# Optimization experiments

Measured on AMD Instinct MI355X. Metric: run time of the kernel, lower is better.

Reference implementation:

```python
import jax, jax.numpy as jnp
import numpy as np

NUM_EMBEDDINGS = 8192
EMB_CHANNELS = 8
BETA = 0.25


def setup_inputs() -> dict:
    key = jax.random.key(0)
    k1, k2 = jax.random.split(key)
    z = jax.random.normal(k1, (8, EMB_CHANNELS, 64, 64), dtype=jnp.float32)
    # torch init: uniform(-1/K, 1/K)
    lim = 1.0 / NUM_EMBEDDINGS
    codebook = jax.random.uniform(
        k2, (NUM_EMBEDDINGS, EMB_CHANNELS), dtype=jnp.float32,
        minval=-lim, maxval=lim)
    return {"z": z, "codebook": codebook}


def reference(z, codebook):
    # z: [B, C, H, W]; codebook: [K, C]
    C = codebook.shape[1]
    z_ch = jnp.moveaxis(z, 1, -1)                 # [B, H, W, C]
    z_flat = z_ch.reshape(-1, C)                  # [N, C]
    # squared-euclidean distances via sum-of-squares + matmul: [N, K]
    dist = (
        jnp.sum(z_flat ** 2, axis=1, keepdims=True)
        + jnp.sum(codebook ** 2, axis=1)
        - 2.0 * jnp.einsum('nd,kd->nk', z_flat, codebook)
    )
    idx = jnp.argmin(dist, axis=1)                # [N]
    z_q = codebook[idx].reshape(z_ch.shape)       # [B, H, W, C]
    z_q = jnp.moveaxis(z_q, -1, 1)                # [B, C, H, W]
    sg = jax.lax.stop_gradient
    loss = (BETA * jnp.mean((sg(z_q) - z) ** 2)
            + jnp.mean((z_q - sg(z)) ** 2))
    # straight-through estimator
    z_q_st = z + sg(z_q - z)
    return z_q_st, loss
```

## Files before the change

kernel.cpp:

```cpp
#include <hip/hip_runtime.h>

typedef __attribute__((ext_vector_type(8))) short short8;
typedef __attribute__((ext_vector_type(4))) float f32x4;

#define NROWS 32768
#define NELEM 262144
#define KCB   8192
#define ROWS_PB 128
#define NWAVE 16

static __device__ __forceinline__ short to_bf16(float x) {
    unsigned u = __float_as_uint(x);
    unsigned r = (u + 0x7FFFu + ((u >> 16) & 1u)) >> 16;
    return (short)r;
}

__global__ __launch_bounds__(256) void vq_prep(
    const float* __restrict__ z, const float* __restrict__ cb,
    short8* __restrict__ cbb, short8* __restrict__ pka, float* __restrict__ out)
{
    int gid = blockIdx.x * 256 + threadIdx.x;
    if (gid == 0) out[NELEM] = 0.0f;
    if (gid < KCB) {
        const float4* p = (const float4*)(cb + (size_t)gid * 8);
        float4 a = p[0], b = p[1];
        float h = -0.5f * (a.x*a.x + a.y*a.y + a.z*a.z + a.w*a.w
                         + b.x*b.x + b.y*b.y + b.z*b.z + b.w*b.w);
        short8 lo = { to_bf16(a.x), to_bf16(a.y), to_bf16(a.z), to_bf16(a.w),
                      to_bf16(b.x), to_bf16(b.y), to_bf16(b.z), to_bf16(b.w) };
        short8 hi = { to_bf16(h), 0, 0, 0, 0, 0, 0, 0 };
        cbb[2 * gid]     = lo;
        cbb[2 * gid + 1] = hi;
    } else {
        int n = gid - KCB;
        int bb = n >> 12, hw = n & 4095;
        const float* zp = z + (size_t)bb * 32768 + hw;
        short8 v = { to_bf16(zp[0]),     to_bf16(zp[4096]),
                     to_bf16(zp[8192]),  to_bf16(zp[12288]),
                     to_bf16(zp[16384]), to_bf16(zp[20480]),
                     to_bf16(zp[24576]), to_bf16(zp[28672]) };
        pka[n] = v;
    }
}

__global__ __launch_bounds__(1024, 4) void vq_main(
    const float* __restrict__ z, const float* __restrict__ cb,
    const short8* __restrict__ cbb, const short8* __restrict__ pka,
    float* __restrict__ out)
{
    __shared__ float sbest[NWAVE][ROWS_PB];
    __shared__ float lsum[NWAVE];

    const int tid  = threadIdx.x;
    const int lane = tid & 63;
    const int w    = tid >> 6;
    const int col  = lane & 15;
    const int g    = lane >> 4;

    const int row0 = blockIdx.x * ROWS_PB;

    short8 af[8];
    #pragma unroll
    for (int f = 0; f < 8; ++f) {
        short8 v = {0, 0, 0, 0, 0, 0, 0, 0};
        if (g == 0)      v = pka[row0 + f * 16 + col];
        else if (g == 1) v[0] = (short)0x3F80;
        af[f] = v;
    }

    const int kbase = w * (KCB / NWAVE);
    const char* bpc = (const char*)cbb + (size_t)(kbase + col) * 32
                                       + (size_t)(g & 1) * 16;

    float best[8][4];
    #pragma unroll
    for (int f = 0; f < 8; ++f)
        #pragma unroll
        for (int r = 0; r < 4; ++r)
            best[f][r] = __uint_as_float(0xFF800000u);

    const unsigned inv0 = (unsigned)(8191 - (kbase + col));
    const f32x4 zacc = {0.f, 0.f, 0.f, 0.f};

#define LDT(T) (*(const short8*)(bpc + (size_t)(T) * 512))

    auto comp = [&](short8 bf, int t) {
        unsigned iv = inv0 - (unsigned)(t * 16);
        #pragma unroll
        for (int f = 0; f < 8; ++f) {
            f32x4 acc = __builtin_amdgcn_mfma_f32_16x16x32_bf16(af[f], bf, zacc, 0, 0, 0);
            #pragma unroll
            for (int r = 0; r < 4; ++r) {
                float p = __uint_as_float((__float_as_uint(acc[r]) & 0xFFFFE000u) | iv);
                best[f][r] = fmaxf(best[f][r], p);
            }
        }
    };

    short8 c0 = LDT(0);
    short8 c1 = LDT(1);
    #pragma unroll
    for (int tt = 0; tt < 16; ++tt) {
        short8 n0, n1;
        if (tt < 15) { n0 = LDT(2 * tt + 2); n1 = LDT(2 * tt + 3); }
        comp(c0, 2 * tt);
        comp(c1, 2 * tt + 1);
        if (tt < 15) { c0 = n0; c1 = n1; }
    }

    #pragma unroll
    for (int d = 1; d < 16; d <<= 1)
        #pragma unroll
        for (int f = 0; f < 8; ++f)
            #pragma unroll
            for (int r = 0; r < 4; ++r)
                best[f][r] = fmaxf(best[f][r], __shfl_xor(best[f][r], d));

    if (col == 0) {
        #pragma unroll
        for (int f = 0; f < 8; ++f)
            #pragma unroll
            for (int r = 0; r < 4; ++r)
                sbest[w][f * 16 + g * 4 + r] = best[f][r];
    }
    __syncthreads();

    const int pos = tid & 127;
    const int ch  = tid >> 7;
    float m = sbest[0][pos];
    #pragma unroll
    for (int kw = 1; kw < NWAVE; ++kw) m = fmaxf(m, sbest[kw][pos]);
    const int k = 8191 - (int)(__float_as_uint(m) & 8191u);

    const int n = row0 + pos;
    const size_t o = ((size_t)(n >> 12)) * 32768 + (size_t)ch * 4096 + (size_t)(n & 4095);
    float ev = cb[(size_t)k * 8 + ch];
    float zz = z[o];
    out[o] = ev;
    float dd = ev - zz;
    float sq = dd * dd;
    #pragma unroll
    for (int off = 32; off > 0; off >>= 1) sq += __shfl_down(sq, off);
    if (lane == 0) lsum[w] = sq;
    __syncthreads();
    if (tid == 0) {
        float s = 0.f;
        #pragma unroll
        for (int kw = 0; kw < NWAVE; ++kw) s += lsum[kw];
        atomicAdd(out + NELEM, s * (1.25f / (float)NELEM));
    }
}

extern "C" void kernel_launch(void* const* d_in, const int* in_sizes, int n_in,
                              void* d_out, int out_size, void* d_ws, size_t ws_size,
                              hipStream_t stream)
{
    const float* z  = (const float*)d_in[0];
    const float* cb = (const float*)d_in[1];
    float* out = (float*)d_out;
    short8* cbb = (short8*)d_ws;
    short8* pka = (short8*)((char*)d_ws + 256 * 1024);

    vq_prep<<<(KCB + NROWS) / 256, 256, 0, stream>>>(z, cb, cbb, pka, out);
    vq_main<<<NROWS / ROWS_PB, 1024, 0, stream>>>(z, cb, cbb, pka, out);
}
```

Before: 39.48 us.

## Switch VQ distance scan to 32x32x16 MFMA with fused and-or/max3 argmax

Replaces the 16x16x32 MFMA tiling, where half of each A operand was padding, with 32x32x16 MFMAs. The codebook is re-laid out in 32-entry blocks that carry separate low and high K halves, so the A operand holds 32 rows plus a bias column and the MFMA produces more useful output per instruction. The argmax packing now uses inline v_and_or_b32 and v_max3_f32 to halve the compare-and-max instruction count per pair of tiles. Blocks shrink to 32 rows and 8 waves, giving 1024 blocks instead of 256. Each block therefore reloads the whole codebook for fewer rows, which means less reuse and more L2 traffic.

```diff
diff --git a/kernel.cpp b/kernel.cpp
--- a/kernel.cpp
+++ b/kernel.cpp
@@ -1,13 +1,13 @@
 #include <hip/hip_runtime.h>
 
 typedef __attribute__((ext_vector_type(8))) short short8;
-typedef __attribute__((ext_vector_type(4))) float f32x4;
+typedef __attribute__((ext_vector_type(16))) float f32x16;
 
 #define NROWS 32768
 #define NELEM 262144
 #define KCB   8192
-#define ROWS_PB 128
-#define NWAVE 16
+#define ROWS_PB 32
+#define NWAVE 8
 
 static __device__ __forceinline__ short to_bf16(float x) {
     unsigned u = __float_as_uint(x);
@@ -17,7 +17,7 @@
 
 __global__ __launch_bounds__(256) void vq_prep(
     const float* __restrict__ z, const float* __restrict__ cb,
-    short8* __restrict__ cbb, short8* __restrict__ pka, float* __restrict__ out)
+    short8* __restrict__ cbb32, short8* __restrict__ pka, float* __restrict__ out)
 {
     int gid = blockIdx.x * 256 + threadIdx.x;
     if (gid == 0) out[NELEM] = 0.0f;
@@ -29,8 +29,8 @@
         short8 lo = { to_bf16(a.x), to_bf16(a.y), to_bf16(a.z), to_bf16(a.w),
                       to_bf16(b.x), to_bf16(b.y), to_bf16(b.z), to_bf16(b.w) };
         short8 hi = { to_bf16(h), 0, 0, 0, 0, 0, 0, 0 };
-        cbb[2 * gid]     = lo;
-        cbb[2 * gid + 1] = hi;
+        cbb32[(gid >> 5) * 64 + (gid & 31)]      = lo;
+        cbb32[(gid >> 5) * 64 + 32 + (gid & 31)] = hi;
     } else {
         int n = gid - KCB;
         int bb = n >> 12, hw = n & 4095;
@@ -43,9 +43,21 @@
     }
 }
 
-__global__ __launch_bounds__(1024, 4) void vq_main(
+static __device__ __forceinline__ void packmax3(float& best, float s0, float s1,
+                                                unsigned iv0, unsigned iv1)
+{
+    float p0, p1;
+    asm("v_and_or_b32 %0, %1, %2, %3"
+        : "=v"(p0) : "v"(s0), "s"(0xFFFFE000u), "v"(iv0));
+    asm("v_and_or_b32 %0, %1, %2, %3"
+        : "=v"(p1) : "v"(s1), "s"(0xFFFFE000u), "v"(iv1));
+    asm("v_max3_f32 %0, %1, %2, %0"
+        : "+v"(best) : "v"(p0), "v"(p1));
+}
+
+__global__ __launch_bounds__(512, 4) void vq_scan32(
     const float* __restrict__ z, const float* __restrict__ cb,
-    const short8* __restrict__ cbb, const short8* __restrict__ pka,
+    const short8* __restrict__ cbb32, const short8* __restrict__ pka,
     float* __restrict__ out)
 {
     __shared__ float sbest[NWAVE][ROWS_PB];
@@ -54,91 +66,79 @@
     const int tid  = threadIdx.x;
     const int lane = tid & 63;
     const int w    = tid >> 6;
-    const int col  = lane & 15;
-    const int g    = lane >> 4;
+    const int c32  = lane & 31;
+    const int hi   = lane >> 5;
 
     const int row0 = blockIdx.x * ROWS_PB;
 
-    short8 af[8];
-    #pragma unroll
-    for (int f = 0; f < 8; ++f) {
-        short8 v = {0, 0, 0, 0, 0, 0, 0, 0};
-        if (g == 0)      v = pka[row0 + f * 16 + col];
-        else if (g == 1) v[0] = (short)0x3F80;
-        af[f] = v;
+    short8 af;
+    if (hi == 0) {
+        af = pka[row0 + c32];
+    } else {
+        short8 one = {(short)0x3F80, 0, 0, 0, 0, 0, 0, 0};
+        af = one;
     }
 
     const int kbase = w * (KCB / NWAVE);
-    const char* bpc = (const char*)cbb + (size_t)(kbase + col) * 32
-                                       + (size_t)(g & 1) * 16;
+    const char* bpc = (const char*)cbb32 + (size_t)kbase * 32
+                    + (size_t)c32 * 16 + (size_t)hi * 512;
 
-    float best[8][4];
+    float best[16];
     #pragma unroll
-    for (int f = 0; f < 8; ++f)
+    for (int r = 0; r < 16; ++r)
+        best[r] = __uint_as_float(0xFF800000u);
+
+    const unsigned inv0 = 8191u - (unsigned)kbase - (unsigned)c32;
+    const f32x16 z16 = {0.f,0.f,0.f,0.f,0.f,0.f,0.f,0.f,
+                        0.f,0.f,0.f,0.f,0.f,0.f,0.f,0.f};
+
+    #pragma unroll 4
+    for (int pr = 0; pr < 16; ++pr) {
+        const char* p = bpc + (size_t)pr * 2048;
+        short8 b0 = *(const short8*)(p);
+        short8 b1 = *(const short8*)(p + 1024);
+        f32x16 d0 = __builtin_amdgcn_mfma_f32_32x32x16_bf16(af, b0, z16, 0, 0, 0);
+        f32x16 d1 = __builtin_amdgcn_mfma_f32_32x32x16_bf16(af, b1, z16, 0, 0, 0);
+        const unsigned iv0 = inv0 - (unsigned)(pr * 64);
+        const unsigned iv1 = iv0 - 32u;
         #pragma unroll
-        for (int r = 0; r < 4; ++r)
-            best[f][r] = __uint_as_float(0xFF800000u);
-
-    const unsigned inv0 = (unsigned)(8191 - (kbase + col));
-    const f32x4 zacc = {0.f, 0.f, 0.f, 0.f};
-
-#define LDT(T) (*(const short8*)(bpc + (size_t)(T) * 512))
-
-    auto comp = [&](short8 bf, int t) {
-        unsigned iv = inv0 - (unsigned)(t * 16);
-        #pragma unroll
-        for (int f = 0; f < 8; ++f) {
-            f32x4 acc = __builtin_amdgcn_mfma_f32_16x16x32_bf16(af[f], bf, zacc, 0, 0, 0);
-            #pragma unroll
-            for (int r = 0; r < 4; ++r) {
-                float p = __uint_as_float((__float_as_uint(acc[r]) & 0xFFFFE000u) | iv);
-                best[f][r] = fmaxf(best[f][r], p);
-            }
-        }
-    };
-
-    short8 c0 = LDT(0);
-    short8 c1 = LDT(1);
-    #pragma unroll
-    for (int tt = 0; tt < 16; ++tt) {
-        short8 n0, n1;
-        if (tt < 15) { n0 = LDT(2 * tt + 2); n1 = LDT(2 * tt + 3); }
-        comp(c0, 2 * tt);
-        comp(c1, 2 * tt + 1);
-        if (tt < 15) { c0 = n0; c1 = n1; }
+        for (int r = 0; r < 16; ++r)
+            packmax3(best[r], d0[r], d1[r], iv0, iv1);
     }
 
     #pragma unroll
-    for (int d = 1; d < 16; d <<= 1)
+    for (int d = 1; d < 32; d <<= 1)
         #pragma unroll
-        for (int f = 0; f < 8; ++f)
-            #pragma unroll
-            for (int r = 0; r < 4; ++r)
-                best[f][r] = fmaxf(best[f][r], __shfl_xor(best[f][r], d));
+        for (int r = 0; r < 16; ++r)
+            best[r] = fmaxf(best[r], __shfl_xor(best[r], d));
 
-    if (col == 0) {
+    if (c32 == 0) {
         #pragma unroll
-        for (int f = 0; f < 8; ++f)
-            #pragma unroll
-            for (int r = 0; r < 4; ++r)
-                sbest[w][f * 16 + g * 4 + r] = best[f][r];
+        for (int r = 0; r < 16; ++r) {
+            const int m = (r & 3) + ((r >> 2) << 3) + (hi << 2);
+            sbest[w][m] = best[r];
+        }
     }
     __syncthreads();
 
-    const int pos = tid & 127;
-    const int ch  = tid >> 7;
-    float m = sbest[0][pos];
-    #pragma unroll
-    for (int kw = 1; kw < NWAVE; ++kw) m = fmaxf(m, sbest[kw][pos]);
-    const int k = 8191 - (int)(__float_as_uint(m) & 8191u);
+    float sq = 0.0f;
+    if (tid < 256) {
+        const int pos = tid & 31;
+        const int ch  = tid >> 5;
+        float m = sbest[0][pos];
+        #pragma unroll
+        for (int kw = 1; kw < NWAVE; ++kw) m = fmaxf(m, sbest[kw][pos]);
+        const int k = 8191 - (int)(__float_as_uint(m) & 8191u);
 
-    const int n = row0 + pos;
-    const size_t o = ((size_t)(n >> 12)) * 32768 + (size_t)ch * 4096 + (size_t)(n & 4095);
-    float ev = cb[(size_t)k * 8 + ch];
-    float zz = z[o];
-    out[o] = ev;
-    float dd = ev - zz;
-    float sq = dd * dd;
+        const int n = row0 + pos;
+        const size_t o = ((size_t)(n >> 12)) * 32768 + (size_t)ch * 4096
+                       + (size_t)(n & 4095);
+        float ev = cb[(size_t)k * 8 + ch];
+        float zz = z[o];
+        out[o] = ev;
+        float dd = ev - zz;
+        sq = dd * dd;
+    }
     #pragma unroll
     for (int off = 32; off > 0; off >>= 1) sq += __shfl_down(sq, off);
     if (lane == 0) lsum[w] = sq;
@@ -158,9 +158,9 @@
     const float* z  = (const float*)d_in[0];
     const float* cb = (const float*)d_in[1];
     float* out = (float*)d_out;
-    short8* cbb = (short8*)d_ws;
-    short8* pka = (short8*)((char*)d_ws + 256 * 1024);
+    short8* cbb32 = (short8*)d_ws;
+    short8* pka   = (short8*)((char*)d_ws + 256 * 1024);
 
-    vq_prep<<<(KCB + NROWS) / 256, 256, 0, stream>>>(z, cb, cbb, pka, out);
-    vq_main<<<NROWS / ROWS_PB, 1024, 0, stream>>>(z, cb, cbb, pka, out);
+    vq_prep<<<(KCB + NROWS) / 256, 256, 0, stream>>>(z, cb, cbb32, pka, out);
+    vq_scan32<<<NROWS / ROWS_PB, 512, 0, stream>>>(z, cb, cbb32, pka, out);
 }
```

Result: faster. 35.65 us (-9.7%).
